# Optimization experiments

Hardware: AMD Instinct MI355X
Metric: run time of the kernel (lower is better)

The kernel has to match this reference:

```python
import jax, jax.numpy as jnp
import numpy as np
import math

D_MODEL = 1024
EXPAND = 2
D_INNER = D_MODEL * EXPAND          # 2048
D_STATE = 16
NHEADS = 8
NGROUPS = 1
D_CONV = 4
HEADDIM = D_INNER // NHEADS         # 256
CONV_DIM = D_INNER + 2 * NGROUPS * D_STATE   # x, B, C go through the causal conv
D_IN_PROJ = 2 * D_INNER + 2 * NGROUPS * D_STATE + NHEADS  # z, xBC, dt
CHUNK = 64
BATCH = 4
SEQLEN = 4096


def setup_inputs() -> dict:
    key = jax.random.key(0)
    ks = jax.random.split(key, 6)
    rng = np.random.default_rng(0)
    u = jax.random.normal(ks[0], (BATCH, SEQLEN, D_MODEL), dtype=jnp.float32)
    W_in = jax.random.normal(ks[1], (D_MODEL, D_IN_PROJ), dtype=jnp.float32) * 0.02
    conv_w = jax.random.normal(ks[2], (CONV_DIM, D_CONV), dtype=jnp.float32) * (1.0 / math.sqrt(D_CONV))
    conv_b = jnp.zeros((CONV_DIM,), dtype=jnp.float32)
    # dt_bias = inverse-softplus of dt sampled log-uniform in [dt_min, dt_max]
    dt = np.exp(rng.uniform(size=NHEADS) * (math.log(0.1) - math.log(0.001)) + math.log(0.001))
    dt = np.clip(dt, 1e-4, None)
    dt_bias = jnp.asarray(dt + np.log(-np.expm1(-dt)), dtype=jnp.float32)
    # A in A_init_range=(0.9, 0.999), stored as A_log with A = -exp(A_log)
    A_log = jnp.asarray(np.log(rng.uniform(0.9, 0.999, NHEADS)), dtype=jnp.float32)
    D = jnp.ones((NHEADS,), dtype=jnp.float32)
    norm_w = jnp.ones((D_INNER,), dtype=jnp.float32)
    W_out = jax.random.normal(ks[3], (D_INNER, D_MODEL), dtype=jnp.float32) * 0.02
    return {"u": u, "W_in": W_in, "conv_w": conv_w, "conv_b": conv_b,
            "dt_bias": dt_bias, "A_log": A_log, "D": D, "norm_w": norm_w, "W_out": W_out}


def _mamba2_fwd(u, W_in, conv_w, conv_b, dt_bias, A_log, D, norm_w, W_out):
    b, l, _ = u.shape
    h, p, n, g, Q = NHEADS, HEADDIM, D_STATE, NGROUPS, CHUNK
    zxbcdt = u @ W_in                                   # [b,l,2*d_inner+2gn+h]
    z = zxbcdt[..., :D_INNER]
    xBC = zxbcdt[..., D_INNER:D_INNER + CONV_DIM]
    dt = jax.nn.softplus(zxbcdt[..., D_INNER + CONV_DIM:] + dt_bias)  # [b,l,h]
    # causal depthwise conv over time (d_conv taps) + SiLU
    xp = jnp.pad(xBC, ((0, 0), (D_CONV - 1, 0), (0, 0)))
    xconv = conv_b
    for k in range(D_CONV):
        xconv = xconv + xp[:, k:k + l, :] * conv_w[:, k]
    xBC = jax.nn.silu(xconv)
    x = xBC[..., :D_INNER].reshape(b, l, h, p)
    B = xBC[..., D_INNER:D_INNER + g * n].reshape(b, l, g, n)
    C = xBC[..., D_INNER + g * n:].reshape(b, l, g, n)
    Bh = jnp.repeat(B, h // g, axis=2)                  # [b,l,h,n]
    Ch = jnp.repeat(C, h // g, axis=2)
    A = -jnp.exp(A_log)                                 # [h]
    # ---- chunked (SSD) selective scan ----
    nc = l // Q
    xc = x.reshape(b, nc, Q, h, p)
    dtc = dt.reshape(b, nc, Q, h)
    Bc = Bh.reshape(b, nc, Q, h, n)
    Cc = Ch.reshape(b, nc, Q, h, n)
    a = dtc * A                                         # [b,nc,Q,h]
    cs = jnp.cumsum(a, axis=2).transpose(0, 1, 3, 2)    # [b,nc,h,Q]
    mask = jnp.tril(jnp.ones((Q, Q), dtype=bool))
    L = jnp.where(mask, jnp.exp(cs[..., :, None] - cs[..., None, :]), 0.0)  # [b,nc,h,Q,Q]
    xdt = xc * dtc[..., None]                           # x scaled by dt
    Y_diag = jnp.einsum('bcqhn,bcshn,bchqs,bcshp->bcqhp', Cc, Bc, L, xdt)
    decay_states = jnp.exp(cs[..., -1:] - cs)           # [b,nc,h,Q]
    states = jnp.einsum('bcqhn,bchq,bcqhp->bchpn', Bc, decay_states, xdt)  # per-chunk state
    chunk_decay = jnp.exp(cs[..., -1])                  # [b,nc,h]
    def step(carry, inp):
        st, dec = inp
        new = dec[..., None, None] * carry + st
        return new, carry
    init = jnp.zeros((b, h, p, n), dtype=u.dtype)
    _, prev = jax.lax.scan(step, init, (states.transpose(1, 0, 2, 3, 4), chunk_decay.transpose(1, 0, 2)))
    prev = prev.transpose(1, 0, 2, 3, 4)                # state entering each chunk [b,nc,h,p,n]
    Y_off = jnp.einsum('bcqhn,bchpn,bchq->bcqhp', Cc, prev, jnp.exp(cs))
    y = (Y_diag + Y_off).reshape(b, l, h, p) + D[:, None] * x
    y = y.reshape(b, l, D_INNER)
    # gated RMSNorm then out projection
    y = y * jax.nn.silu(z)
    y = y * jax.lax.rsqrt(jnp.mean(y * y, axis=-1, keepdims=True) + 1e-5) * norm_w
    return y @ W_out


def reference(u, W_in, conv_w, conv_b, dt_bias, A_log, D, norm_w, W_out):
    return _mamba2_fwd(u, W_in, conv_w, conv_b, dt_bias, A_log, D, norm_w, W_out)
```

## Files before the change

kernel.cpp:

```cpp
#include <hip/hip_runtime.h>
#include <cstddef>
#include <cstdint>
#include <type_traits>

constexpr int DM = 1024;
constexpr int DI = 2048;
constexpr int DS = 16;
constexpr int NH = 8;
constexpr int CD = 2080;
constexpr int DP = 4136;
constexpr int DPT = 4224;
constexpr int Q  = 64;
constexpr int B_ = 4;
constexpr int L_ = 4096;
constexpr int NCH = 64;
constexpr int HP = 256;
constexpr int NR = B_ * L_;

constexpr size_t AL(size_t x) { return (x + 255) & ~(size_t)255; }
constexpr size_t OFFB_ZX = 0;
constexpr size_t OFFB_BC = AL(OFFB_ZX + (size_t)NR * DP * 2);
constexpr size_t OFFB_DT = AL(OFFB_BC + (size_t)NR * 32 * 4);
constexpr size_t OFFB_CS = AL(OFFB_DT + (size_t)NR * NH * 4);
constexpr size_t OFFB_ST = AL(OFFB_CS + (size_t)B_ * NCH * NH * Q * 4);
constexpr size_t OFFB_Y  = AL(OFFB_ST + (size_t)B_ * NCH * NH * HP * DS * 4);
constexpr size_t OFFB_WO = AL(OFFB_Y + (size_t)NR * DI * 2);

__device__ __forceinline__ float silu_f(float x) { return x / (1.f + expf(-x)); }
__device__ __forceinline__ float bf2f(unsigned short v) {
  unsigned int u = ((unsigned int)v) << 16;
  return __builtin_bit_cast(float, u);
}
__device__ __forceinline__ unsigned short f2bf(float f) {
  unsigned int u = __builtin_bit_cast(unsigned int, f);
  u += 0x7FFFu + ((u >> 16) & 1u);
  return (unsigned short)(u >> 16);
}

typedef __attribute__((ext_vector_type(8))) short bf16x8;
typedef __attribute__((ext_vector_type(4))) float f32x4;

template<bool OUT_BF16>
__global__ __launch_bounds__(256)
void gemm_mfma(const unsigned short* __restrict__ A, const unsigned short* __restrict__ Bt,
               void* __restrict__ Cout, int M, int N, int K, int ldc) {
  __shared__ unsigned short As[128 * 64];
  __shared__ unsigned short Bs[128 * 64];
  const int t = threadIdx.x;
  const int w = t >> 6, l = t & 63;
  const int quad = l >> 4, lan = l & 15;
  const int wm = w >> 1, wn = w & 1;
  const int row0 = blockIdx.y * 128, col0 = blockIdx.x * 128;

  f32x4 acc[4][4];
  #pragma unroll
  for (int i = 0; i < 4; ++i)
    #pragma unroll
    for (int j = 0; j < 4; ++j)
      acc[i][j] = (f32x4)(0.0f);

  for (int k0 = 0; k0 < K; k0 += 64) {
    __syncthreads();
    #pragma unroll
    for (int i = 0; i < 4; ++i) {
      const int jc = i * 256 + w * 64 + l;
      const int m = jc >> 3, c8 = jc & 7;
      const int gc8 = c8 ^ (m & 7);
      const unsigned short* gp = A + (size_t)(row0 + m) * K + k0 + (gc8 << 3);
      unsigned short* lp = &As[(size_t)(i * 256 + w * 64) * 8];
      __builtin_amdgcn_global_load_lds((const __attribute__((address_space(1))) void*)gp,
                                       (__attribute__((address_space(3))) void*)lp, 16, 0, 0);
    }
    #pragma unroll
    for (int i = 0; i < 4; ++i) {
      const int jc = i * 256 + w * 64 + l;
      const int n = jc >> 3, c8 = jc & 7;
      const int gc8 = c8 ^ (n & 7);
      const unsigned short* gp = Bt + (size_t)(col0 + n) * K + k0 + (gc8 << 3);
      unsigned short* lp = &Bs[(size_t)(i * 256 + w * 64) * 8];
      __builtin_amdgcn_global_load_lds((const __attribute__((address_space(1))) void*)gp,
                                       (__attribute__((address_space(3))) void*)lp, 16, 0, 0);
    }
    __syncthreads();
    #pragma unroll
    for (int kk = 0; kk < 64; kk += 32) {
      const int kc = quad + (kk >> 3);
      bf16x8 af[4], bf[4];
      #pragma unroll
      for (int mi = 0; mi < 4; ++mi) {
        const int m = wm * 64 + mi * 16 + lan;
        af[mi] = *(const bf16x8*)&As[m * 64 + ((kc ^ (m & 7)) << 3)];
      }
      #pragma unroll
      for (int ni = 0; ni < 4; ++ni) {
        const int n = wn * 64 + ni * 16 + lan;
        bf[ni] = *(const bf16x8*)&Bs[n * 64 + ((kc ^ (n & 7)) << 3)];
      }
      #pragma unroll
      for (int mi = 0; mi < 4; ++mi)
        #pragma unroll
        for (int ni = 0; ni < 4; ++ni)
          acc[mi][ni] = __builtin_amdgcn_mfma_f32_16x16x32_bf16(af[mi], bf[ni], acc[mi][ni], 0, 0, 0);
    }
  }
  #pragma unroll
  for (int mi = 0; mi < 4; ++mi) {
    const size_t rb = row0 + wm * 64 + mi * 16 + quad * 4;
    #pragma unroll
    for (int ni = 0; ni < 4; ++ni) {
      const int colb = col0 + wn * 64 + ni * 16 + lan;
      if (colb < N) {
        if constexpr (OUT_BF16) {
          unsigned short* C = (unsigned short*)Cout;
          #pragma unroll
          for (int r = 0; r < 4; ++r)
            C[(rb + r) * (size_t)ldc + colb] = f2bf(acc[mi][ni][r]);
        } else {
          float* C = (float*)Cout;
          #pragma unroll
          for (int r = 0; r < 4; ++r)
            C[(rb + r) * (size_t)ldc + colb] = acc[mi][ni][r];
        }
      }
    }
  }
}

__global__ __launch_bounds__(256)
void cvt_bf16(const float* __restrict__ src, unsigned short* __restrict__ dst, size_t n4) {
  const size_t i = ((size_t)blockIdx.x * 256 + threadIdx.x) * 4;
  if (i < n4 * 4) {
    float4 v = *(const float4*)(src + i);
    ushort4 o;
    o.x = f2bf(v.x); o.y = f2bf(v.y); o.z = f2bf(v.z); o.w = f2bf(v.w);
    *(ushort4*)(dst + i) = o;
  }
}

__global__ __launch_bounds__(256)
void transpose_cvt(const float* __restrict__ src, unsigned short* __restrict__ dst,
                   int R, int C, int Cvalid) {
  __shared__ float T[64][65];
  const int t = threadIdx.x;
  const int n0 = blockIdx.x * 64, k0 = blockIdx.y * 64;
  #pragma unroll
  for (int i = 0; i < 4; ++i) {
    int f = t + i * 256;
    int r = f >> 4, c4 = (f & 15) << 2;
    int n = n0 + c4;
    float4 v = make_float4(0.f, 0.f, 0.f, 0.f);
    if (n + 3 < Cvalid) {
      v = *(const float4*)(src + (size_t)(k0 + r) * C + n);
    } else {
      if (n + 0 < Cvalid) v.x = src[(size_t)(k0 + r) * C + n + 0];
      if (n + 1 < Cvalid) v.y = src[(size_t)(k0 + r) * C + n + 1];
      if (n + 2 < Cvalid) v.z = src[(size_t)(k0 + r) * C + n + 2];
      if (n + 3 < Cvalid) v.w = src[(size_t)(k0 + r) * C + n + 3];
    }
    T[r][c4 + 0] = v.x; T[r][c4 + 1] = v.y; T[r][c4 + 2] = v.z; T[r][c4 + 3] = v.w;
  }
  __syncthreads();
  #pragma unroll
  for (int i = 0; i < 4; ++i) {
    int f = t + i * 256;
    int c = f >> 4, r4 = (f & 15) << 2;
    ushort4 o;
    o.x = f2bf(T[r4 + 0][c]); o.y = f2bf(T[r4 + 1][c]);
    o.z = f2bf(T[r4 + 2][c]); o.w = f2bf(T[r4 + 3][c]);
    *(ushort4*)(dst + (size_t)(n0 + c) * R + k0 + r4) = o;
  }
}

__global__ __launch_bounds__(256)
void convbc_kernel(const unsigned short* __restrict__ zx, const float* __restrict__ cw,
                   const float* __restrict__ cb, float* __restrict__ bc) {
  const int idx = blockIdx.x * 256 + threadIdx.x;
  const int j = idx & 31;
  const int row = idx >> 5;
  const int l = row & (L_ - 1);
  const int cc = DI + j;
  float a = cb[cc];
  #pragma unroll
  for (int k = 0; k < 4; ++k) {
    int ll = l - 3 + k;
    if (ll >= 0)
      a += bf2f(zx[(size_t)(row - 3 + k) * DP + (DI + DI + j)]) * cw[cc * 4 + k];
  }
  bc[(size_t)row * 32 + j] = silu_f(a);
}

__global__ __launch_bounds__(256)
void dt_kernel(const unsigned short* __restrict__ zx, const float* __restrict__ dt_bias,
               float* __restrict__ dt) {
  const int i = blockIdx.x * 256 + threadIdx.x;
  const int h = i & 7;
  const size_t row = (size_t)(i >> 3);
  float x = bf2f(zx[row * DP + (DI + CD) + h]) + dt_bias[h];
  dt[i] = (x > 20.f) ? x : log1pf(expf(x));
}

__global__ __launch_bounds__(256)
void chunk_kernel(const unsigned short* __restrict__ zx, const float* __restrict__ bc,
                  const float* __restrict__ dt, const float* __restrict__ A_log,
                  const float* __restrict__ cw, const float* __restrict__ cb,
                  const float* __restrict__ Dp, float* __restrict__ cs_out,
                  float* __restrict__ states, unsigned short* __restrict__ yb) {
  const int c = blockIdx.x, h = blockIdx.y, b = blockIdx.z;
  const int t = threadIdx.x;
  __shared__ float dtS[Q], csS[Q], ddS[Q];
  __shared__ __align__(16) float BsS[Q][DS], CsS[Q][DS];
  __shared__ __align__(16) float Msd[Q][Q + 4];
  __shared__ __align__(16) float xs[Q][Q + 4];
  __shared__ __align__(16) unsigned short rawS[Q + 3][Q];
  const size_t rowb = (size_t)b * L_ + (size_t)c * Q;

  if (t < Q) dtS[t] = dt[(rowb + t) * NH + h];
  __syncthreads();
  if (t == 0) {
    float A = -expf(A_log[h]);
    float s = 0.f;
    for (int q = 0; q < Q; ++q) { s += dtS[q] * A; csS[q] = s; }
  }
  __syncthreads();
  if (t < Q) {
    ddS[t] = expf(csS[Q - 1] - csS[t]) * dtS[t];
    cs_out[(((size_t)b * NCH + c) * NH + h) * Q + t] = csS[t];
  }
  for (int i = t; i < Q * DS; i += 256) {
    int q = i >> 4, n = i & 15;
    BsS[q][n] = bc[(rowb + q) * 32 + n];
    CsS[q][n] = bc[(rowb + q) * 32 + 16 + n];
  }
  __syncthreads();
  const float Dh = Dp[h];
  for (int i = t; i < Q * Q; i += 256) {
    int q = i >> 6, s = i & 63;
    float v = 0.f;
    if (s <= q) {
      float d = 0.f;
      #pragma unroll
      for (int n = 0; n < DS; ++n) d += CsS[q][n] * BsS[s][n];
      v = expf(csS[q] - csS[s]) * d * dtS[s];
      if (s == q) v += Dh;
    }
    Msd[q][s] = v;
  }
  __syncthreads();

  const int qg = t >> 4, pg = t & 15;
  const int ps = t & 63, n4 = t >> 6;
  const int pch = t & 63, qb0 = t >> 6;

  for (int pt = 0; pt < 4; ++pt) {
    const int col0 = DI + h * HP + pt * Q;
    for (int v = t; v < 67 * 8; v += 256) {
      int i = v >> 3, p0 = (v & 7) * 8;
      int lg = c * Q - 3 + i;
      uint4 val = make_uint4(0, 0, 0, 0);
      if (lg >= 0)
        val = *(const uint4*)(zx + ((size_t)b * L_ + lg) * DP + col0 + p0);
      *(uint4*)&rawS[i][p0] = val;
    }
    __syncthreads();
    {
      const int cc = h * HP + pt * Q + pch;
      const float w0 = cw[cc * 4 + 0], w1 = cw[cc * 4 + 1];
      const float w2 = cw[cc * 4 + 2], w3 = cw[cc * 4 + 3];
      const float bias = cb[cc];
      #pragma unroll
      for (int i2 = 0; i2 < 16; ++i2) {
        int q = qb0 + 4 * i2;
        float a = bias + bf2f(rawS[q][pch]) * w0 + bf2f(rawS[q + 1][pch]) * w1
                       + bf2f(rawS[q + 2][pch]) * w2 + bf2f(rawS[q + 3][pch]) * w3;
        xs[q][pch] = silu_f(a);
      }
    }
    __syncthreads();
    {
      float a0 = 0, a1 = 0, a2 = 0, a3 = 0;
      for (int q = 0; q < Q; ++q) {
        float w = xs[q][ps] * ddS[q];
        a0 += w * BsS[q][n4 * 4 + 0];
        a1 += w * BsS[q][n4 * 4 + 1];
        a2 += w * BsS[q][n4 * 4 + 2];
        a3 += w * BsS[q][n4 * 4 + 3];
      }
      size_t sb = ((((size_t)b * NCH + c) * NH + h) * HP + pt * Q + ps) * DS + n4 * 4;
      *(float4*)(states + sb) = make_float4(a0, a1, a2, a3);
    }
    {
      float acc[4][4] = {};
      for (int s0 = 0; s0 < Q; s0 += 4) {
        float xr[4][4], mr[4][4];
        #pragma unroll
        for (int k = 0; k < 4; ++k) *(float4*)xr[k] = *(const float4*)&xs[s0 + k][pg * 4];
        #pragma unroll
        for (int i = 0; i < 4; ++i) *(float4*)mr[i] = *(const float4*)&Msd[qg * 4 + i][s0];
        #pragma unroll
        for (int i = 0; i < 4; ++i)
          #pragma unroll
          for (int k = 0; k < 4; ++k)
            #pragma unroll
            for (int j = 0; j < 4; ++j)
              acc[i][j] += mr[i][k] * xr[k][j];
      }
      #pragma unroll
      for (int i = 0; i < 4; ++i) {
        size_t row = rowb + qg * 4 + i;
        ushort4 o;
        o.x = f2bf(acc[i][0]); o.y = f2bf(acc[i][1]);
        o.z = f2bf(acc[i][2]); o.w = f2bf(acc[i][3]);
        *(ushort4*)(yb + row * DI + h * HP + pt * Q + pg * 4) = o;
      }
    }
    __syncthreads();
  }
}

__global__ __launch_bounds__(256)
void scan_kernel(float* __restrict__ states, const float* __restrict__ cs) {
  const int pn = blockIdx.x * 256 + threadIdx.x;
  const int h = blockIdx.y, b = blockIdx.z;
  const size_t cstride = (size_t)NH * HP * DS;
  const size_t base = ((size_t)b * NCH * NH + h) * (size_t)(HP * DS) + pn;
  float carry = 0.f;
  for (int c = 0; c < NCH; ++c) {
    float dec = expf(cs[(((size_t)b * NCH + c) * NH + h) * Q + (Q - 1)]);
    float st = states[base + (size_t)c * cstride];
    states[base + (size_t)c * cstride] = carry;
    carry = dec * carry + st;
  }
}

__global__ __launch_bounds__(256)
void yoff_kernel(const float* __restrict__ bc, const float* __restrict__ cs,
                 const float* __restrict__ prev, unsigned short* __restrict__ yb) {
  const int c = blockIdx.x, h = blockIdx.y, b = blockIdx.z;
  const int t = threadIdx.x;
  __shared__ __align__(16) float CsS[Q][DS];
  __shared__ float ecs[Q];
  const size_t rowb = (size_t)b * L_ + (size_t)c * Q;
  const size_t pb = (((size_t)b * NCH + c) * NH + h) * (size_t)(HP * DS);
  for (int i = t; i < Q * DS; i += 256) {
    int q = i >> 4, n = i & 15;
    CsS[q][n] = bc[(rowb + q) * 32 + 16 + n];
  }
  if (t < Q) ecs[t] = expf(cs[(((size_t)b * NCH + c) * NH + h) * Q + t]);
  float pv[16];
  #pragma unroll
  for (int k = 0; k < 4; ++k)
    *(float4*)&pv[k * 4] = *(const float4*)(prev + pb + (size_t)t * DS + k * 4);
  __syncthreads();
  for (int q = 0; q < Q; ++q) {
    float acc = 0.f;
    #pragma unroll
    for (int n = 0; n < DS; ++n) acc += CsS[q][n] * pv[n];
    const size_t idx = (rowb + q) * DI + h * HP + t;
    yb[idx] = f2bf(bf2f(yb[idx]) + ecs[q] * acc);
  }
}

__global__ __launch_bounds__(256)
void gatenorm_kernel(const unsigned short* __restrict__ zx, const float* __restrict__ norm_w,
                     unsigned short* __restrict__ yb) {
  const size_t row = blockIdx.x;
  const int t = threadIdx.x;
  const unsigned short* zrow = zx + row * DP;
  unsigned short* yrow = yb + row * DI;
  const int d0 = t * 8;
  uint4 yv = *(const uint4*)(yrow + d0);
  uint4 zv = *(const uint4*)(zrow + d0);
  const unsigned short* ys = (const unsigned short*)&yv;
  const unsigned short* zs = (const unsigned short*)&zv;
  float v[8];
  float ss = 0.f;
  #pragma unroll
  for (int j = 0; j < 8; ++j) {
    float val = bf2f(ys[j]) * silu_f(bf2f(zs[j]));
    v[j] = val;
    ss += val * val;
  }
  #pragma unroll
  for (int off = 32; off > 0; off >>= 1) ss += __shfl_down(ss, off);
  __shared__ float red[4];
  if ((t & 63) == 0) red[t >> 6] = ss;
  __syncthreads();
  float tot = red[0] + red[1] + red[2] + red[3];
  float scale = rsqrtf(tot / (float)DI + 1e-5f);
  ushort4 o[2];
  unsigned short* op = (unsigned short*)o;
  #pragma unroll
  for (int j = 0; j < 8; ++j) op[j] = f2bf(v[j] * scale * norm_w[d0 + j]);
  *(uint4*)(yrow + d0) = *(uint4*)o;
}

extern "C" void kernel_launch(void* const* d_in, const int* in_sizes, int n_in,
                              void* d_out, int out_size, void* d_ws, size_t ws_size,
                              hipStream_t stream) {
  const float* u       = (const float*)d_in[0];
  const float* W_in    = (const float*)d_in[1];
  const float* conv_w  = (const float*)d_in[2];
  const float* conv_b  = (const float*)d_in[3];
  const float* dt_bias = (const float*)d_in[4];
  const float* A_log   = (const float*)d_in[5];
  const float* Dp      = (const float*)d_in[6];
  const float* norm_w  = (const float*)d_in[7];
  const float* W_out   = (const float*)d_in[8];
  float* out = (float*)d_out;
  char* w = (char*)d_ws;

  unsigned short* zx  = (unsigned short*)(w + OFFB_ZX);
  float* bcb          = (float*)(w + OFFB_BC);
  float* dtb          = (float*)(w + OFFB_DT);
  float* csb          = (float*)(w + OFFB_CS);
  float* stb          = (float*)(w + OFFB_ST);
  unsigned short* yb  = (unsigned short*)(w + OFFB_Y);
  unsigned short* ub  = (unsigned short*)(w + OFFB_ST);
  unsigned short* wib = (unsigned short*)(w + OFFB_Y);
  unsigned short* wob = (unsigned short*)(w + OFFB_WO);

  cvt_bf16<<<(NR * DM / 4 + 255) / 256, 256, 0, stream>>>(u, ub, (size_t)NR * DM / 4);
  transpose_cvt<<<dim3(DPT / 64, DM / 64), 256, 0, stream>>>(W_in, wib, DM, DP, DP);
  transpose_cvt<<<dim3(DM / 64, DI / 64), 256, 0, stream>>>(W_out, wob, DI, DM, DM);
  gemm_mfma<true><<<dim3(DPT / 128, NR / 128), 256, 0, stream>>>(
      ub, wib, zx, NR, DP, DM, DP);
  convbc_kernel<<<(NR * 32) / 256, 256, 0, stream>>>(zx, conv_w, conv_b, bcb);
  dt_kernel<<<(NR * NH) / 256, 256, 0, stream>>>(zx, dt_bias, dtb);
  chunk_kernel<<<dim3(NCH, NH, B_), 256, 0, stream>>>(zx, bcb, dtb, A_log, conv_w,
                                                      conv_b, Dp, csb, stb, yb);
  scan_kernel<<<dim3((HP * DS) / 256, NH, B_), 256, 0, stream>>>(stb, csb);
  yoff_kernel<<<dim3(NCH, NH, B_), 256, 0, stream>>>(bcb, csb, stb, yb);
  gatenorm_kernel<<<NR, 256, 0, stream>>>(zx, norm_w, yb);
  gemm_mfma<false><<<dim3(DM / 128, NR / 128), 256, 0, stream>>>(
      yb, wob, out, NR, DM, DI, DM);
}
```

Measured before the change: 662.1 us.

## Use bf16 MFMA for intra-chunk diagonal output and chunk state computation

```diff
diff --git a/kernel.cpp b/kernel.cpp
--- a/kernel.cpp
+++ b/kernel.cpp
@@ -207,10 +207,14 @@
                   float* __restrict__ states, unsigned short* __restrict__ yb) {
   const int c = blockIdx.x, h = blockIdx.y, b = blockIdx.z;
   const int t = threadIdx.x;
+  const int w = t >> 6, l = t & 63;
+  const int quad = l >> 4, lan = l & 15;
   __shared__ float dtS[Q], csS[Q], ddS[Q];
-  __shared__ __align__(16) float BsS[Q][DS], CsS[Q][DS];
-  __shared__ __align__(16) float Msd[Q][Q + 4];
-  __shared__ __align__(16) float xs[Q][Q + 4];
+  __shared__ float BsS[Q][DS + 1];
+  __shared__ float CsS[Q][DS];
+  __shared__ __align__(16) unsigned short Msd[Q][Q + 8];
+  __shared__ __align__(16) unsigned short BdT[DS][Q + 8];
+  __shared__ __align__(16) unsigned short xsT[Q][Q + 8];
   __shared__ __align__(16) unsigned short rawS[Q + 3][Q];
   const size_t rowb = (size_t)b * L_ + (size_t)c * Q;
 
@@ -232,6 +236,10 @@
     CsS[q][n] = bc[(rowb + q) * 32 + 16 + n];
   }
   __syncthreads();
+  for (int i = t; i < DS * Q; i += 256) {
+    int n = i & 15, q = i >> 4;
+    BdT[n][q] = f2bf(BsS[q][n] * ddS[q]);
+  }
   const float Dh = Dp[h];
   for (int i = t; i < Q * Q; i += 256) {
     int q = i >> 6, s = i & 63;
@@ -243,12 +251,9 @@
       v = expf(csS[q] - csS[s]) * d * dtS[s];
       if (s == q) v += Dh;
     }
-    Msd[q][s] = v;
-  }
-  __syncthreads();
-
-  const int qg = t >> 4, pg = t & 15;
-  const int ps = t & 63, n4 = t >> 6;
+    Msd[q][s] = f2bf(v);
+  }
+
   const int pch = t & 63, qb0 = t >> 6;
 
   for (int pt = 0; pt < 4; ++pt) {
@@ -272,45 +277,41 @@
         int q = qb0 + 4 * i2;
         float a = bias + bf2f(rawS[q][pch]) * w0 + bf2f(rawS[q + 1][pch]) * w1
                        + bf2f(rawS[q + 2][pch]) * w2 + bf2f(rawS[q + 3][pch]) * w3;
-        xs[q][pch] = silu_f(a);
+        xsT[pch][q] = f2bf(silu_f(a));
       }
     }
     __syncthreads();
+    bf16x8 xfrag[2];
+    #pragma unroll
+    for (int ks = 0; ks < 2; ++ks)
+      xfrag[ks] = *(const bf16x8*)&xsT[w * 16 + lan][quad * 8 + ks * 32];
     {
-      float a0 = 0, a1 = 0, a2 = 0, a3 = 0;
-      for (int q = 0; q < Q; ++q) {
-        float w = xs[q][ps] * ddS[q];
-        a0 += w * BsS[q][n4 * 4 + 0];
-        a1 += w * BsS[q][n4 * 4 + 1];
-        a2 += w * BsS[q][n4 * 4 + 2];
-        a3 += w * BsS[q][n4 * 4 + 3];
-      }
-      size_t sb = ((((size_t)b * NCH + c) * NH + h) * HP + pt * Q + ps) * DS + n4 * 4;
-      *(float4*)(states + sb) = make_float4(a0, a1, a2, a3);
+      f32x4 sacc = (f32x4)(0.0f);
+      #pragma unroll
+      for (int ks = 0; ks < 2; ++ks) {
+        bf16x8 bfr = *(const bf16x8*)&BdT[lan][quad * 8 + ks * 32];
+        sacc = __builtin_amdgcn_mfma_f32_16x16x32_bf16(xfrag[ks], bfr, sacc, 0, 0, 0);
+      }
+      const int p = w * 16 + quad * 4;
+      const size_t sb = ((((size_t)b * NCH + c) * NH + h) * HP + pt * Q + p) * DS + lan;
+      #pragma unroll
+      for (int r = 0; r < 4; ++r)
+        states[sb + (size_t)r * DS] = sacc[r];
     }
     {
-      float acc[4][4] = {};
-      for (int s0 = 0; s0 < Q; s0 += 4) {
-        float xr[4][4], mr[4][4];
+      #pragma unroll
+      for (int mi = 0; mi < 4; ++mi) {
+        f32x4 yac = (f32x4)(0.0f);
         #pragma unroll
-        for (int k = 0; k < 4; ++k) *(float4*)xr[k] = *(const float4*)&xs[s0 + k][pg * 4];
+        for (int ks = 0; ks < 2; ++ks) {
+          bf16x8 am = *(const bf16x8*)&Msd[mi * 16 + lan][quad * 8 + ks * 32];
+          yac = __builtin_amdgcn_mfma_f32_16x16x32_bf16(am, xfrag[ks], yac, 0, 0, 0);
+        }
+        const int qrow = mi * 16 + quad * 4;
+        const int pcol = h * HP + pt * Q + w * 16 + lan;
         #pragma unroll
-        for (int i = 0; i < 4; ++i) *(float4*)mr[i] = *(const float4*)&Msd[qg * 4 + i][s0];
-        #pragma unroll
-        for (int i = 0; i < 4; ++i)
-          #pragma unroll
-          for (int k = 0; k < 4; ++k)
-            #pragma unroll
-            for (int j = 0; j < 4; ++j)
-              acc[i][j] += mr[i][k] * xr[k][j];
-      }
-      #pragma unroll
-      for (int i = 0; i < 4; ++i) {
-        size_t row = rowb + qg * 4 + i;
-        ushort4 o;
-        o.x = f2bf(acc[i][0]); o.y = f2bf(acc[i][1]);
-        o.z = f2bf(acc[i][2]); o.w = f2bf(acc[i][3]);
-        *(ushort4*)(yb + row * DI + h * HP + pt * Q + pg * 4) = o;
+        for (int r = 0; r < 4; ++r)
+          yb[(rowb + qrow + r) * (size_t)DI + pcol] = f2bf(yac[r]);
       }
     }
     __syncthreads();
```

Result: faster. 578.8 us (-12.6%).
